# Kernel optimization log

Hardware: AMD Instinct MI355X
Metric: run time of the kernel (lower is better)

Reference implementation:

```python
import jax, jax.numpy as jnp
import numpy as np
import math

H = 768
NH = 12
DK = H // NH
EPS = 1e-12

def gelu(x):
    return 0.5 * x * (1 + jnp.tanh(math.sqrt(2 / math.pi) * (x + 0.044715 * x ** 3)))

def layernorm(x, w, b):
    u = x.mean(-1, keepdims=True)
    s = ((x - u) ** 2).mean(-1, keepdims=True)
    return w * (x - u) / jnp.sqrt(s + EPS) + b

def setup_inputs() -> dict:
    key = jax.random.key(0)
    ks = jax.random.split(key, 12)
    B, S = 4, 2048
    std = 1.0 / math.sqrt(H)
    inp = {
        'x': jax.random.normal(ks[0], (B, S, H), jnp.float32),
        'mask': jax.random.randint(ks[1], (B, S), 0, 2, jnp.int32),
        'wq': jax.random.normal(ks[2], (H, H), jnp.float32) * std,
        'wk': jax.random.normal(ks[3], (H, H), jnp.float32) * std,
        'wv': jax.random.normal(ks[4], (H, H), jnp.float32) * std,
        'wo': jax.random.normal(ks[5], (H, H), jnp.float32) * std,
        'wo_b': jnp.zeros((H,), jnp.float32),
        'w1': jax.random.normal(ks[6], (H, 4 * H), jnp.float32) * std,
        'w1_b': jnp.zeros((4 * H,), jnp.float32),
        'w2': jax.random.normal(ks[7], (4 * H, H), jnp.float32) * (0.5 / math.sqrt(H)),
        'w2_b': jnp.zeros((H,), jnp.float32),
        'ln1_w': jnp.ones((H,), jnp.float32),
        'ln1_b': jnp.zeros((H,), jnp.float32),
        'ln2_w': jnp.ones((H,), jnp.float32),
        'ln2_b': jnp.zeros((H,), jnp.float32),
    }
    return inp

def reference(x, mask, wq, wk, wv, wo, wo_b, w1, w1_b, w2, w2_b, ln1_w, ln1_b, ln2_w, ln2_b):
    B, S, _ = x.shape
    # --- attention sublayer (pre-LN, residual) ---
    y = layernorm(x, ln1_w, ln1_b)
    q = (y @ wq).reshape(B, S, NH, DK).transpose(0, 2, 1, 3)
    k = (y @ wk).reshape(B, S, NH, DK).transpose(0, 2, 1, 3)
    v = (y @ wv).reshape(B, S, NH, DK).transpose(0, 2, 1, 3)
    scores = jnp.einsum('bhqd,bhkd->bhqk', q, k) / math.sqrt(DK)
    m2 = (mask[:, :, None] * mask[:, None, :])[:, None, :, :]  # [B,1,S,S]
    scores = jnp.where(m2 == 0, jnp.float32(-1e9), scores)
    p = jax.nn.softmax(scores, axis=-1)
    ctx = jnp.einsum('bhqk,bhkd->bhqd', p, v).transpose(0, 2, 1, 3).reshape(B, S, H)
    x = x + ctx @ wo + wo_b
    # --- FFN sublayer ---
    y2 = layernorm(x, ln2_w, ln2_b)
    x = x + gelu(y2 @ w1 + w1_b) @ w2 + w2_b
    return x
```

## Files before the change

### kernel.cpp

```cpp
#include <hip/hip_runtime.h>
#include <hip/hip_bf16.h>

#define HD   768
#define BSZ  4
#define SEQ  2048
#define NTOK (BSZ*SEQ)
#define NHD  12
#define DKD  64

typedef __bf16 bf16_t;
typedef __bf16 bf16x8 __attribute__((ext_vector_type(8)));
typedef __bf16 bf16x4 __attribute__((ext_vector_type(4)));
typedef float  f32x4  __attribute__((ext_vector_type(4)));

__device__ __forceinline__ void async16(const void* g, void* l) {
    __builtin_amdgcn_global_load_lds(
        (const __attribute__((address_space(1))) unsigned int*)g,
        (__attribute__((address_space(3))) unsigned int*)l, 16, 0, 0);
}

__global__ __launch_bounds__(256) void wconv_kernel(
    const float* __restrict__ in, bf16_t* __restrict__ out, int K, int N)
{
    __shared__ float tile[32][33];
    const int k0 = blockIdx.y * 32, n0 = blockIdx.x * 32;
    const int t = threadIdx.x, r = t >> 5, c = t & 31;
#pragma unroll
    for (int j = 0; j < 4; j++)
        tile[r + 8*j][c] = in[(size_t)(k0 + r + 8*j) * N + n0 + c];
    __syncthreads();
#pragma unroll
    for (int j = 0; j < 4; j++)
        out[(size_t)(n0 + r + 8*j) * K + k0 + c] = (bf16_t)tile[c][r + 8*j];
}

__global__ __launch_bounds__(256) void mbias_kernel(
    const int* __restrict__ mask, float* __restrict__ mb)
{
    const int i = blockIdx.x * 256 + threadIdx.x;
    mb[i] = mask[i] ? 0.f : -1e9f;
}

__global__ __launch_bounds__(256) void ln_kernel(
    const float* __restrict__ x, const float* __restrict__ gw,
    const float* __restrict__ gb, bf16_t* __restrict__ y)
{
    const int row = blockIdx.x, t = threadIdx.x;
    const float* xr = x + (size_t)row * HD;
    float v0 = xr[t], v1 = xr[t + 256], v2 = xr[t + 512];
    float s1 = v0 + v1 + v2;
    float s2 = v0*v0 + v1*v1 + v2*v2;
#pragma unroll
    for (int m = 1; m < 64; m <<= 1) {
        s1 += __shfl_xor(s1, m);
        s2 += __shfl_xor(s2, m);
    }
    __shared__ float red[8];
    const int w = t >> 6, l = t & 63;
    if (l == 0) { red[w] = s1; red[4 + w] = s2; }
    __syncthreads();
    s1 = red[0] + red[1] + red[2] + red[3];
    s2 = red[4] + red[5] + red[6] + red[7];
    float mean = s1 * (1.f/HD);
    float var  = fmaxf(s2 * (1.f/HD) - mean*mean, 0.f);
    float rstd = rsqrtf(var + 1e-12f);
    bf16_t* yr = y + (size_t)row * HD;
    yr[t]       = (bf16_t)(gw[t]      * (v0 - mean) * rstd + gb[t]);
    yr[t + 256] = (bf16_t)(gw[t + 256]* (v1 - mean) * rstd + gb[t + 256]);
    yr[t + 512] = (bf16_t)(gw[t + 512]* (v2 - mean) * rstd + gb[t + 512]);
}

template<int EPI>
__global__ __launch_bounds__(256) void gemm_bt(
    const bf16_t* __restrict__ A, const bf16_t* __restrict__ BT,
    const float* __restrict__ bias, const float* __restrict__ resid,
    void* __restrict__ outv, int M, int N, int K, int ldo)
{
    __shared__ __align__(16) unsigned char lds[49152];
    const int t = threadIdx.x;
    const int w = t >> 6, l = t & 63;
    const int wr = w >> 1, wc = w & 1;
    const int lr = l & 15, lg = l >> 4;
    const int nwg = gridDim.x * gridDim.y;
    int flat = blockIdx.y * gridDim.x + blockIdx.x;
    flat = (flat & 7) * (nwg >> 3) + (flat >> 3);
    const int bx = flat % gridDim.x, by = flat / gridDim.x;
    const int m0 = by * 128, n0 = bx * 128;

    const bf16_t* a_src = A  + (size_t)(m0 + (t >> 2)) * K + (t & 3) * 8;
    const bf16_t* b_src = BT + (size_t)(n0 + (t >> 2)) * K + (t & 3) * 8;
    f32x4 acc[4][4] = {};

    auto stage = [&](int kt, int buf) {
        unsigned char* d = lds + buf * 16384 + t * 16;
        async16(a_src + kt,                 d);
        async16(a_src + (size_t)64*K + kt,  d + 4096);
        async16(b_src + kt,                 d + 8192);
        async16(b_src + (size_t)64*K + kt,  d + 12288);
    };

    const int nt = K >> 5;
    stage(0, 0);
    stage(32, 1);
    asm volatile("s_waitcnt vmcnt(4)" ::: "memory");
    __builtin_amdgcn_s_barrier();

    int cur = 0;
    for (int it = 0; it < nt; ++it) {
        const bool pre = (it + 2 < nt);
        if (pre) {
            int b2 = cur + 2; if (b2 >= 3) b2 -= 3;
            stage((it + 2) << 5, b2);
        }
        const unsigned char* bufp = lds + cur * 16384;
        bf16x8 af[4], bfr[4];
#pragma unroll
        for (int n = 0; n < 4; n++)
            bfr[n] = *(const bf16x8*)(bufp + 8192 + (wc*64 + n*16 + lr)*64 + lg*16);
#pragma unroll
        for (int m = 0; m < 4; m++)
            af[m] = *(const bf16x8*)(bufp + (wr*64 + m*16 + lr)*64 + lg*16);
        __builtin_amdgcn_s_setprio(1);
#pragma unroll
        for (int m = 0; m < 4; m++)
#pragma unroll
            for (int n = 0; n < 4; n++)
                acc[m][n] = __builtin_amdgcn_mfma_f32_16x16x32_bf16(af[m], bfr[n], acc[m][n], 0, 0, 0);
        __builtin_amdgcn_s_setprio(0);
        if (it + 1 < nt) {
            asm volatile("s_waitcnt lgkmcnt(0)" ::: "memory");
            if (pre) asm volatile("s_waitcnt vmcnt(4)" ::: "memory");
            else     asm volatile("s_waitcnt vmcnt(0)" ::: "memory");
            __builtin_amdgcn_s_barrier();
        }
        cur = (cur + 1 == 3) ? 0 : cur + 1;
    }

#pragma unroll
    for (int m = 0; m < 4; m++) {
#pragma unroll
        for (int n = 0; n < 4; n++) {
#pragma unroll
            for (int i = 0; i < 4; i++) {
                const int gr = m0 + wr*64 + m*16 + lg*4 + i;
                const int gc = n0 + wc*64 + n*16 + lr;
                float v = acc[m][n][i];
                if constexpr (EPI == 0) {
                    ((bf16_t*)outv)[(size_t)gr * ldo + gc] = (bf16_t)v;
                } else if constexpr (EPI == 1) {
                    ((float*)outv)[(size_t)gr * ldo + gc] =
                        v + bias[gc] + resid[(size_t)gr * ldo + gc];
                } else {
                    v += bias[gc];
                    float u = 0.7978845608028654f * (v + 0.044715f * v * v * v);
                    float g = v / (1.f + __expf(-2.f * u));
                    ((bf16_t*)outv)[(size_t)gr * ldo + gc] = (bf16_t)g;
                }
            }
        }
    }
}

__global__ __launch_bounds__(256) void vtrans_kernel(
    const bf16_t* __restrict__ qkv, bf16_t* __restrict__ vt)
{
    const int bh = blockIdx.y, b = bh / NHD, h = bh % NHD;
    const int s0 = blockIdx.x * 64;
    __shared__ bf16_t tile[64][72];
    const int t = threadIdx.x;
    {
        const int r = t >> 2, c0 = (t & 3) * 16;
        const bf16_t* src = qkv + (size_t)(b*SEQ + s0 + r) * 2304 + 1536 + h*64 + c0;
#pragma unroll
        for (int j = 0; j < 16; j++) tile[r][c0 + j] = src[j];
    }
    __syncthreads();
    {
        const int d = t >> 2, j0 = (t & 3) * 16;
        bf16_t* dst = vt + ((size_t)bh*64 + d) * SEQ + s0 + j0;
#pragma unroll
        for (int j = 0; j < 16; j++) dst[j] = tile[j0 + j][d];
    }
}

__global__ __launch_bounds__(256) void attn_kernel(
    const bf16_t* __restrict__ qkv, const bf16_t* __restrict__ vt,
    const int* __restrict__ mask, const float* __restrict__ mbias,
    bf16_t* __restrict__ ctx)
{
    __shared__ __align__(16) unsigned char lds[49152];
    const int t = threadIdx.x, w = t >> 6, l = t & 63;
    const int lr = l & 15, lg = l >> 4;
    int flat = blockIdx.y * 16 + blockIdx.x;
    flat = (flat & 7) * 96 + (flat >> 3);
    const int bh = flat >> 4, qt = flat & 15;
    const int b = bh / NHD, h = bh % NHD;
    const int q0 = qt * 128 + w * 32;
    const int swz = (lr & 7) << 4;

    bf16x8 qf[2][2];
#pragma unroll
    for (int r = 0; r < 2; r++)
#pragma unroll
        for (int ks = 0; ks < 2; ks++)
            qf[r][ks] = *(const bf16x8*)(qkv + (size_t)(b*SEQ + q0 + r*16 + lr)*2304
                                         + h*64 + ks*32 + lg*8);
    int mq[2];
#pragma unroll
    for (int r = 0; r < 2; r++)
        mq[r] = mask[b*SEQ + q0 + r*16 + lr];

    float mrow[2] = { -INFINITY, -INFINITY };
    float lsum[2] = { 0.f, 0.f };
    f32x4 accO[2][4] = {};

    auto stage_kv = [&](int kt, int buf) {
        unsigned char* d = lds + buf * 16384;
#pragma unroll
        for (int i2 = 0; i2 < 2; i2++) {
            const int c = i2*256 + t;
            const int row = c >> 3;
            const int scol = ((c & 7) ^ (row & 7)) * 8;
            async16(qkv + (size_t)(b*SEQ + kt + row)*2304 + 768 + h*64 + scol,
                    d + c*16);
            async16(vt + ((size_t)bh*64 + row)*SEQ + kt + scol,
                    d + 8192 + c*16);
        }
    };

    stage_kv(0, 0);
    __syncthreads();

    int cur = 0;
    for (int kt = 0; kt < SEQ; kt += 64) {
        if (kt + 64 < SEQ) stage_kv(kt + 64, cur ^ 1);
        f32x4 mb[4];
#pragma unroll
        for (int n = 0; n < 4; n++)
            mb[n] = *(const f32x4*)(mbias + (size_t)b*SEQ + kt + n*16 + lg*4);
        const unsigned char* bufp = lds + cur * 16384;

        bf16x8 kf[4][2];
#pragma unroll
        for (int n = 0; n < 4; n++)
#pragma unroll
            for (int ks = 0; ks < 2; ks++)
                kf[n][ks] = *(const bf16x8*)(bufp + (n*16 + lr)*128
                                             + ((ks*64 + lg*16) ^ swz));
        f32x4 accS[4][2] = {};
        __builtin_amdgcn_s_setprio(1);
#pragma unroll
        for (int n = 0; n < 4; n++)
#pragma unroll
            for (int r = 0; r < 2; r++)
#pragma unroll
                for (int ks = 0; ks < 2; ks++)
                    accS[n][r] = __builtin_amdgcn_mfma_f32_16x16x32_bf16(
                        kf[n][ks], qf[r][ks], accS[n][r], 0, 0, 0);
        __builtin_amdgcn_s_setprio(0);

#pragma unroll
        for (int r = 0; r < 2; r++) {
            f32x4 sl[4];
#pragma unroll
            for (int n = 0; n < 4; n++)
#pragma unroll
                for (int i = 0; i < 4; i++)
                    sl[n][i] = mq[r] ? (accS[n][r][i] * 0.125f + mb[n][i]) : -1e9f;
            float px = -INFINITY;
#pragma unroll
            for (int n = 0; n < 4; n++)
                px = fmaxf(px, fmaxf(fmaxf(sl[n][0], sl[n][1]),
                                     fmaxf(sl[n][2], sl[n][3])));
            px = fmaxf(px, __shfl_xor(px, 16));
            px = fmaxf(px, __shfl_xor(px, 32));
            const float mold = mrow[r];
            if (!__all(px <= mold + 8.f)) {
                const float mnew = fmaxf(mold, px);
                const float sc = __expf(mold - mnew);
                lsum[r] *= sc;
#pragma unroll
                for (int dn = 0; dn < 4; dn++) accO[r][dn] *= sc;
                mrow[r] = mnew;
            }
            const float m = mrow[r];
            float ps = 0.f;
#pragma unroll
            for (int n = 0; n < 4; n++) {
                bf16x4 pk;
#pragma unroll
                for (int i = 0; i < 4; i++) {
                    float pv = __expf(sl[n][i] - m);
                    ps += pv;
                    pk[i] = (bf16_t)pv;
                }
                *(bf16x4*)(lds + 32768 + w*4096 + (r*16 + lr)*128
                           + ((n*32 + lg*8) ^ swz)) = pk;
            }
            ps += __shfl_xor(ps, 16);
            ps += __shfl_xor(ps, 32);
            lsum[r] += ps;
        }

        bf16x8 vf[4][2], pf[2][2];
#pragma unroll
        for (int dn = 0; dn < 4; dn++)
#pragma unroll
            for (int ks = 0; ks < 2; ks++)
                vf[dn][ks] = *(const bf16x8*)(bufp + 8192 + (dn*16 + lr)*128
                                              + ((ks*64 + lg*16) ^ swz));
#pragma unroll
        for (int r = 0; r < 2; r++)
#pragma unroll
            for (int ks = 0; ks < 2; ks++)
                pf[r][ks] = *(const bf16x8*)(lds + 32768 + w*4096 + (r*16 + lr)*128
                                             + ((ks*64 + lg*16) ^ swz));
        __builtin_amdgcn_s_setprio(1);
#pragma unroll
        for (int r = 0; r < 2; r++)
#pragma unroll
            for (int dn = 0; dn < 4; dn++)
#pragma unroll
                for (int ks = 0; ks < 2; ks++)
                    accO[r][dn] = __builtin_amdgcn_mfma_f32_16x16x32_bf16(
                        vf[dn][ks], pf[r][ks], accO[r][dn], 0, 0, 0);
        __builtin_amdgcn_s_setprio(0);

        __syncthreads();
        cur ^= 1;
    }

#pragma unroll
    for (int r = 0; r < 2; r++) {
        const float inv = 1.f / lsum[r];
#pragma unroll
        for (int dn = 0; dn < 4; dn++) {
            bf16x4 ov;
#pragma unroll
            for (int i = 0; i < 4; i++)
                ov[i] = (bf16_t)(accO[r][dn][i] * inv);
            *(bf16x4*)(ctx + (size_t)(b*SEQ + q0 + r*16 + lr)*HD
                       + h*64 + dn*16 + lg*4) = ov;
        }
    }
}

extern "C" void kernel_launch(void* const* d_in, const int* in_sizes, int n_in,
                              void* d_out, int out_size, void* d_ws, size_t ws_size,
                              hipStream_t stream)
{
    const float* x     = (const float*)d_in[0];
    const int*   mask  = (const int*)  d_in[1];
    const float* wq    = (const float*)d_in[2];
    const float* wk    = (const float*)d_in[3];
    const float* wv    = (const float*)d_in[4];
    const float* wo    = (const float*)d_in[5];
    const float* wo_b  = (const float*)d_in[6];
    const float* w1    = (const float*)d_in[7];
    const float* w1_b  = (const float*)d_in[8];
    const float* w2    = (const float*)d_in[9];
    const float* w2_b  = (const float*)d_in[10];
    const float* ln1_w = (const float*)d_in[11];
    const float* ln1_b = (const float*)d_in[12];
    const float* ln2_w = (const float*)d_in[13];
    const float* ln2_b = (const float*)d_in[14];

    unsigned char* ws = (unsigned char*)d_ws;
    size_t o = 0;
    auto alloc = [&](size_t bytes) {
        size_t r = o; o += (bytes + 255) & ~(size_t)255; return r;
    };
    bf16_t* wqkvT = (bf16_t*)(ws + alloc((size_t)2304*768*2));
    bf16_t* woT   = (bf16_t*)(ws + alloc((size_t)768*768*2));
    bf16_t* w1T   = (bf16_t*)(ws + alloc((size_t)3072*768*2));
    bf16_t* w2T   = (bf16_t*)(ws + alloc((size_t)768*3072*2));
    bf16_t* y     = (bf16_t*)(ws + alloc((size_t)NTOK*HD*2));
    float*  x1    = (float*) (ws + alloc((size_t)NTOK*HD*4));
    bf16_t* ctx   = (bf16_t*)(ws + alloc((size_t)NTOK*HD*2));
    float*  mbias = (float*) (ws + alloc((size_t)NTOK*4));
    bf16_t* qkv   = (bf16_t*)(ws + alloc((size_t)NTOK*2304*2));
    bf16_t* vt    = (bf16_t*)(ws + alloc((size_t)48*64*SEQ*2));
    bf16_t* hbuf  = qkv;
    (void)in_sizes; (void)n_in; (void)out_size; (void)ws_size;

    wconv_kernel<<<dim3(24,24),256,0,stream>>>(wq, wqkvT,                 768, 768);
    wconv_kernel<<<dim3(24,24),256,0,stream>>>(wk, wqkvT + 768*768,       768, 768);
    wconv_kernel<<<dim3(24,24),256,0,stream>>>(wv, wqkvT + 2*768*768,     768, 768);
    wconv_kernel<<<dim3(24,24),256,0,stream>>>(wo, woT,                   768, 768);
    wconv_kernel<<<dim3(96,24),256,0,stream>>>(w1, w1T,                   768, 3072);
    wconv_kernel<<<dim3(24,96),256,0,stream>>>(w2, w2T,                   3072, 768);
    mbias_kernel<<<32,256,0,stream>>>(mask, mbias);

    ln_kernel<<<NTOK,256,0,stream>>>(x, ln1_w, ln1_b, y);
    gemm_bt<0><<<dim3(18,64),256,0,stream>>>(y, wqkvT, nullptr, nullptr, qkv,
                                             NTOK, 2304, 768, 2304);
    vtrans_kernel<<<dim3(32,48),256,0,stream>>>(qkv, vt);
    attn_kernel<<<dim3(16,48),256,0,stream>>>(qkv, vt, mask, mbias, ctx);
    gemm_bt<1><<<dim3(6,64),256,0,stream>>>(ctx, woT, wo_b, x, x1,
                                            NTOK, 768, 768, 768);
    ln_kernel<<<NTOK,256,0,stream>>>(x1, ln2_w, ln2_b, y);
    gemm_bt<2><<<dim3(24,64),256,0,stream>>>(y, w1T, w1_b, nullptr, hbuf,
                                             NTOK, 3072, 768, 3072);
    gemm_bt<1><<<dim3(6,64),256,0,stream>>>(hbuf, w2T, w2_b, x1, d_out,
                                            NTOK, 768, 3072, 768);
}
```

Measured before the change: 435.0 us.

## Replace 128x128 GEMM with 256x256 tile, 8-wave, swizzled LDS double-buffered kernel

Replaces the 128x128, 4-wave GEMM with a 256x256 tile, 512-thread kernel that uses a 64-wide K step, an XOR-swizzled LDS layout and double buffering. Loads of A and B for the next step are staged between four MFMA phases, separated by barriers. The goal is more reuse per LDS byte and fewer bank conflicts, improving MFMA utilisation for all four GEMMs. The cost is 128KB of LDS, fewer workgroups (e.g. 96 for the Wo/W2 GEMMs on a 256-CU part), and many extra barriers. The XCD-aware block remap is also changed.

```diff
diff --git a/kernel.cpp b/kernel.cpp
--- a/kernel.cpp
+++ b/kernel.cpp
@@ -71,90 +71,154 @@
 }
 
 template<int EPI>
-__global__ __launch_bounds__(256) void gemm_bt(
+__global__ __launch_bounds__(512, 2) void gemm256(
     const bf16_t* __restrict__ A, const bf16_t* __restrict__ BT,
     const float* __restrict__ bias, const float* __restrict__ resid,
     void* __restrict__ outv, int M, int N, int K, int ldo)
 {
-    __shared__ __align__(16) unsigned char lds[49152];
+    __shared__ __align__(16) unsigned char lds[131072];
     const int t = threadIdx.x;
     const int w = t >> 6, l = t & 63;
-    const int wr = w >> 1, wc = w & 1;
+    const int wm = w >> 2, wn = w & 3;
     const int lr = l & 15, lg = l >> 4;
-    const int nwg = gridDim.x * gridDim.y;
-    int flat = blockIdx.y * gridDim.x + blockIdx.x;
-    flat = (flat & 7) * (nwg >> 3) + (flat >> 3);
-    const int bx = flat % gridDim.x, by = flat / gridDim.x;
-    const int m0 = by * 128, n0 = bx * 128;
-
-    const bf16_t* a_src = A  + (size_t)(m0 + (t >> 2)) * K + (t & 3) * 8;
-    const bf16_t* b_src = BT + (size_t)(n0 + (t >> 2)) * K + (t & 3) * 8;
-    f32x4 acc[4][4] = {};
-
-    auto stage = [&](int kt, int buf) {
-        unsigned char* d = lds + buf * 16384 + t * 16;
-        async16(a_src + kt,                 d);
-        async16(a_src + (size_t)64*K + kt,  d + 4096);
-        async16(b_src + kt,                 d + 8192);
-        async16(b_src + (size_t)64*K + kt,  d + 12288);
+    const int gx = gridDim.x;
+    const int d = blockIdx.y * gx + blockIdx.x;
+    const int xcd = d & 7, jj = d >> 3;
+    const int by = xcd + 8 * (jj / gx), bx = jj % gx;
+    const size_t m0 = (size_t)by * 256, n0 = (size_t)bx * 256;
+
+    const int srow = t >> 3;
+    const int scol = ((t & 7) ^ (srow & 7)) * 8;
+    const bf16_t* a_src = A  + (m0 + srow) * K + scol;
+    const bf16_t* b_src = BT + (n0 + srow) * K + scol;
+
+    auto stageA = [&](int kt, int buf) {
+        unsigned char* dst = lds + buf * 65536 + t * 16;
+#pragma unroll
+        for (int j2 = 0; j2 < 4; j2++)
+            async16(a_src + (size_t)(64 * j2) * K + kt, dst + j2 * 8192);
     };
-
-    const int nt = K >> 5;
-    stage(0, 0);
-    stage(32, 1);
-    asm volatile("s_waitcnt vmcnt(4)" ::: "memory");
+    auto stageB = [&](int kt, int buf) {
+        unsigned char* dst = lds + buf * 65536 + 32768 + t * 16;
+#pragma unroll
+        for (int j2 = 0; j2 < 4; j2++)
+            async16(b_src + (size_t)(64 * j2) * K + kt, dst + j2 * 8192);
+    };
+
+    stageA(0, 0);
+    stageB(0, 0);
+    asm volatile("s_waitcnt vmcnt(0)" ::: "memory");
     __builtin_amdgcn_s_barrier();
 
-    int cur = 0;
+    f32x4 acc[8][4] = {};
+    const int kswz = (lr & 7) << 4;
+    const int nt = K >> 6;
+
     for (int it = 0; it < nt; ++it) {
-        const bool pre = (it + 2 < nt);
-        if (pre) {
-            int b2 = cur + 2; if (b2 >= 3) b2 -= 3;
-            stage((it + 2) << 5, b2);
-        }
-        const unsigned char* bufp = lds + cur * 16384;
-        bf16x8 af[4], bfr[4];
-#pragma unroll
-        for (int n = 0; n < 4; n++)
-            bfr[n] = *(const bf16x8*)(bufp + 8192 + (wc*64 + n*16 + lr)*64 + lg*16);
-#pragma unroll
-        for (int m = 0; m < 4; m++)
-            af[m] = *(const bf16x8*)(bufp + (wr*64 + m*16 + lr)*64 + lg*16);
-        __builtin_amdgcn_s_setprio(1);
-#pragma unroll
-        for (int m = 0; m < 4; m++)
-#pragma unroll
-            for (int n = 0; n < 4; n++)
-                acc[m][n] = __builtin_amdgcn_mfma_f32_16x16x32_bf16(af[m], bfr[n], acc[m][n], 0, 0, 0);
-        __builtin_amdgcn_s_setprio(0);
-        if (it + 1 < nt) {
-            asm volatile("s_waitcnt lgkmcnt(0)" ::: "memory");
-            if (pre) asm volatile("s_waitcnt vmcnt(4)" ::: "memory");
-            else     asm volatile("s_waitcnt vmcnt(0)" ::: "memory");
-            __builtin_amdgcn_s_barrier();
-        }
-        cur = (cur + 1 == 3) ? 0 : cur + 1;
-    }
-
-#pragma unroll
-    for (int m = 0; m < 4; m++) {
-#pragma unroll
-        for (int n = 0; n < 4; n++) {
+        const int cur = it & 1;
+        const unsigned char* Ab = lds + cur * 65536;
+        const unsigned char* Bb = Ab + 32768;
+        const bool pre = (it + 1 < nt);
+        bf16x8 af[4][2], bfr[4][2];
+
+#pragma unroll
+        for (int mi = 0; mi < 4; mi++)
+#pragma unroll
+            for (int ks = 0; ks < 2; ks++)
+                af[mi][ks] = *(const bf16x8*)(Ab + (wm*128 + mi*16 + lr)*128
+                                              + ((ks*64 + lg*16) ^ kswz));
+#pragma unroll
+        for (int ni = 0; ni < 2; ni++)
+#pragma unroll
+            for (int ks = 0; ks < 2; ks++)
+                bfr[ni][ks] = *(const bf16x8*)(Bb + (wn*64 + ni*16 + lr)*128
+                                               + ((ks*64 + lg*16) ^ kswz));
+        if (pre) stageA((it + 1) << 6, cur ^ 1);
+        __builtin_amdgcn_s_barrier();
+        __builtin_amdgcn_s_setprio(1);
+#pragma unroll
+        for (int mi = 0; mi < 4; mi++)
+#pragma unroll
+            for (int ni = 0; ni < 2; ni++)
+#pragma unroll
+                for (int ks = 0; ks < 2; ks++)
+                    acc[mi][ni] = __builtin_amdgcn_mfma_f32_16x16x32_bf16(
+                        af[mi][ks], bfr[ni][ks], acc[mi][ni], 0, 0, 0);
+        __builtin_amdgcn_s_setprio(0);
+        __builtin_amdgcn_s_barrier();
+
+#pragma unroll
+        for (int ni = 2; ni < 4; ni++)
+#pragma unroll
+            for (int ks = 0; ks < 2; ks++)
+                bfr[ni][ks] = *(const bf16x8*)(Bb + (wn*64 + ni*16 + lr)*128
+                                               + ((ks*64 + lg*16) ^ kswz));
+        if (pre) stageB((it + 1) << 6, cur ^ 1);
+        __builtin_amdgcn_s_barrier();
+        __builtin_amdgcn_s_setprio(1);
+#pragma unroll
+        for (int mi = 0; mi < 4; mi++)
+#pragma unroll
+            for (int ni = 2; ni < 4; ni++)
+#pragma unroll
+                for (int ks = 0; ks < 2; ks++)
+                    acc[mi][ni] = __builtin_amdgcn_mfma_f32_16x16x32_bf16(
+                        af[mi][ks], bfr[ni][ks], acc[mi][ni], 0, 0, 0);
+        __builtin_amdgcn_s_setprio(0);
+        __builtin_amdgcn_s_barrier();
+
+#pragma unroll
+        for (int mi = 0; mi < 4; mi++)
+#pragma unroll
+            for (int ks = 0; ks < 2; ks++)
+                af[mi][ks] = *(const bf16x8*)(Ab + (wm*128 + (mi+4)*16 + lr)*128
+                                              + ((ks*64 + lg*16) ^ kswz));
+        __builtin_amdgcn_s_barrier();
+        __builtin_amdgcn_s_setprio(1);
+#pragma unroll
+        for (int mi = 0; mi < 4; mi++)
+#pragma unroll
+            for (int ni = 0; ni < 2; ni++)
+#pragma unroll
+                for (int ks = 0; ks < 2; ks++)
+                    acc[mi+4][ni] = __builtin_amdgcn_mfma_f32_16x16x32_bf16(
+                        af[mi][ks], bfr[ni][ks], acc[mi+4][ni], 0, 0, 0);
+        __builtin_amdgcn_s_setprio(0);
+        __builtin_amdgcn_s_barrier();
+
+        __builtin_amdgcn_s_setprio(1);
+#pragma unroll
+        for (int mi = 0; mi < 4; mi++)
+#pragma unroll
+            for (int ni = 2; ni < 4; ni++)
+#pragma unroll
+                for (int ks = 0; ks < 2; ks++)
+                    acc[mi+4][ni] = __builtin_amdgcn_mfma_f32_16x16x32_bf16(
+                        af[mi][ks], bfr[ni][ks], acc[mi+4][ni], 0, 0, 0);
+        __builtin_amdgcn_s_setprio(0);
+        asm volatile("s_waitcnt vmcnt(0)" ::: "memory");
+        __builtin_amdgcn_s_barrier();
+    }
+
+#pragma unroll
+    for (int mi = 0; mi < 8; mi++) {
+#pragma unroll
+        for (int ni = 0; ni < 4; ni++) {
 #pragma unroll
             for (int i = 0; i < 4; i++) {
-                const int gr = m0 + wr*64 + m*16 + lg*4 + i;
-                const int gc = n0 + wc*64 + n*16 + lr;
-                float v = acc[m][n][i];
+                const size_t gr = m0 + wm*128 + mi*16 + lg*4 + i;
+                const size_t gc = n0 + wn*64 + ni*16 + lr;
+                float v = acc[mi][ni][i];
                 if constexpr (EPI == 0) {
-                    ((bf16_t*)outv)[(size_t)gr * ldo + gc] = (bf16_t)v;
+                    ((bf16_t*)outv)[gr * ldo + gc] = (bf16_t)v;
                 } else if constexpr (EPI == 1) {
-                    ((float*)outv)[(size_t)gr * ldo + gc] =
-                        v + bias[gc] + resid[(size_t)gr * ldo + gc];
+                    ((float*)outv)[gr * ldo + gc] =
+                        v + bias[gc] + resid[gr * ldo + gc];
                 } else {
                     v += bias[gc];
                     float u = 0.7978845608028654f * (v + 0.044715f * v * v * v);
                     float g = v / (1.f + __expf(-2.f * u));
-                    ((bf16_t*)outv)[(size_t)gr * ldo + gc] = (bf16_t)g;
+                    ((bf16_t*)outv)[gr * ldo + gc] = (bf16_t)g;
                 }
             }
         }
@@ -392,15 +456,15 @@
     mbias_kernel<<<32,256,0,stream>>>(mask, mbias);
 
     ln_kernel<<<NTOK,256,0,stream>>>(x, ln1_w, ln1_b, y);
-    gemm_bt<0><<<dim3(18,64),256,0,stream>>>(y, wqkvT, nullptr, nullptr, qkv,
-                                             NTOK, 2304, 768, 2304);
+    gemm256<0><<<dim3(9,32),512,0,stream>>>(y, wqkvT, nullptr, nullptr, qkv,
+                                            NTOK, 2304, 768, 2304);
     vtrans_kernel<<<dim3(32,48),256,0,stream>>>(qkv, vt);
     attn_kernel<<<dim3(16,48),256,0,stream>>>(qkv, vt, mask, mbias, ctx);
-    gemm_bt<1><<<dim3(6,64),256,0,stream>>>(ctx, woT, wo_b, x, x1,
+    gemm256<1><<<dim3(3,32),512,0,stream>>>(ctx, woT, wo_b, x, x1,
                                             NTOK, 768, 768, 768);
     ln_kernel<<<NTOK,256,0,stream>>>(x1, ln2_w, ln2_b, y);
-    gemm_bt<2><<<dim3(24,64),256,0,stream>>>(y, w1T, w1_b, nullptr, hbuf,
+    gemm256<2><<<dim3(12,32),512,0,stream>>>(y, w1T, w1_b, nullptr, hbuf,
                                              NTOK, 3072, 768, 3072);
-    gemm_bt<1><<<dim3(6,64),256,0,stream>>>(hbuf, w2T, w2_b, x1, d_out,
+    gemm256<1><<<dim3(3,32),512,0,stream>>>(hbuf, w2T, w2_b, x1, d_out,
                                             NTOK, 768, 3072, 768);
 }
```

Result: slower. 489.2 us (+12.4%).
